# Optimization experiments

Hardware: AMD Instinct MI355X
Metric: run time of the kernel (lower is better)

## Reference

```python
import jax, jax.numpy as jnp
import numpy as np

B, T_Q, T_K, H = 16, 1024, 1024, 1024


def _linear_params(key, fan_in, fan_out):
    kw, kb = jax.random.split(key)
    bound = 1.0 / np.sqrt(fan_in)
    W = jax.random.uniform(kw, (fan_out, fan_in), jnp.float32, -bound, bound)
    b = jax.random.uniform(kb, (fan_out,), jnp.float32, -bound, bound)
    return W, b


def setup_inputs() -> dict:
    key = jax.random.key(0)
    ks = jax.random.split(key, 6)
    query = jax.random.normal(ks[0], (B, T_Q, H), jnp.float32)
    keys = jax.random.normal(ks[1], (B, T_K, H), jnp.float32)
    values = jax.random.normal(ks[2], (B, T_K, H), jnp.float32)
    Wq, bq = _linear_params(ks[3], H, H)
    Wk, bk = _linear_params(ks[4], H, H)
    Wo, bo = _linear_params(ks[5], H, H)
    return {"query": query, "keys": keys, "values": values,
            "Wq": Wq, "bq": bq, "Wk": Wk, "bk": bk, "Wo": Wo, "bo": bo}


def reference(query, keys, values, Wq, bq, Wk, bk, Wo, bo):
    # Linear projections (torch Linear: x @ W.T + b)
    q = jnp.einsum('bth,oh->bto', query, Wq) + bq   # (B, T_Q, H)
    k = jnp.einsum('bsh,oh->bso', keys, Wk) + bk    # (B, T_K, H)
    # Unscaled scores -> softmax over key axis (dropout is identity at eval)
    scores = jnp.einsum('bto,bso->bts', q, k)       # (B, T_Q, T_K)
    attn = jax.nn.softmax(scores, axis=-1)
    ctx = jnp.einsum('bts,bsh->bth', attn, values)  # note: raw values, value_fc unused in source
    ctx = ctx / jnp.sqrt(jnp.float32(values.shape[1]))
    out = jnp.einsum('bth,oh->bto', ctx, Wo) + bo
    return out
```

## Files before the change

### kernel.cpp

```cpp
#include <hip/hip_runtime.h>
#include <math.h>

typedef __attribute__((ext_vector_type(4))) float f32x4;
typedef __attribute__((ext_vector_type(8))) _Float16 h16x8;
typedef __attribute__((ext_vector_type(4))) short s16x4;

__device__ inline unsigned short f2h(float f) {
    union { _Float16 h; unsigned short u; } v; v.h = (_Float16)f; return v.u;
}

__device__ inline void async16(const void* g, void* l) {
    __builtin_amdgcn_global_load_lds(
        (const __attribute__((address_space(1))) unsigned int*)g,
        (__attribute__((address_space(3))) unsigned int*)l, 16, 0, 0);
}

#define BM 256
#define BN 256
#define BK 64
#define NTHREADS 512


__device__ inline void stage_half(const unsigned short* g, int row0, int kel, int K,
                                  unsigned ldsbase, char* smem, int tid) {
    const int rl  = tid >> 3;
    const int scb = ((tid & 7) ^ (rl & 7)) << 4;
    char* wb = smem + ldsbase + (unsigned)((tid >> 6) << 10);
#pragma unroll
    for (int s = 0; s < 2; ++s) {
        long off = ((long)(row0 + s * 64 + rl) * K + kel) * 2 + scb;
        async16((const char*)g + off, wb + s * 8192);
    }
}

__device__ inline h16x8 ld_frag(const char* smem, unsigned base, int row, int kbyte) {
    unsigned off = base + (unsigned)(row * 128) + (unsigned)(kbyte ^ ((row & 7) << 4));
    return *(const h16x8*)(smem + off);
}

template<int OM>
__global__ __launch_bounds__(NTHREADS, 2)
void gemm256(const unsigned short* __restrict__ A,
             const unsigned short* __restrict__ B,
             const float* __restrict__ bias,
             void* __restrict__ C, int N, int K,
             long sA, long sB, long sC, float scale)
{
    __shared__ __align__(16) char smem[131072];

    const int tid  = threadIdx.x;
    const int wv   = tid >> 6;
    const int lane = tid & 63;
    const int wr = wv >> 2, wc = wv & 3;
    const int lrow = lane & 15;
    const int kq16 = (lane >> 4) * 16;

    const long gx = gridDim.x, gy = gridDim.y;
    const long nwg = gx * gy * (long)gridDim.z;
    const long hw  = ((long)blockIdx.z * gy + blockIdx.y) * gx + blockIdx.x;
    const long qq = nwg >> 3, rr = nwg & 7;
    const long xcd = hw & 7, pos = hw >> 3;
    const long lg = (xcd < rr) ? xcd * (qq + 1) + pos
                               : rr * (qq + 1) + (xcd - rr) * qq + pos;
    const int bx = (int)(lg % gx);
    const long rem = lg / gx;
    const int by = (int)(rem % gy);
    const int bz = (int)(rem / gy);

    const int n0 = bx * BN;
    const int m0 = by * BM;

    const unsigned short* Ag = A + (long)bz * sA;
    const unsigned short* Bg = B + (long)bz * sB;

    const int NT = K / BK;

    auto stageA = [&](int t, int h) {
        stage_half(Ag, m0 + h * 128, t * BK, K,
                   (unsigned)(((t & 1) << 16) + (h << 14)), smem, tid);
    };
    auto stageB = [&](int t, int h) {
        stage_half(Bg, n0 + h * 128, t * BK, K,
                   (unsigned)(((t & 1) << 16) + 32768 + (h << 14)), smem, tid);
    };

    f32x4 acc[8][4];
#pragma unroll
    for (int i = 0; i < 8; ++i)
#pragma unroll
        for (int j = 0; j < 4; ++j) acc[i][j] = (f32x4){0.f, 0.f, 0.f, 0.f};

    const unsigned AbaseW = (unsigned)(wr * 16384);
    const unsigned BbaseW = (unsigned)(32768 + (wc >> 1) * 16384);
    const int brow0 = (wc & 1) * 64;

    stageB(0, 0); stageB(0, 1); stageA(0, 0); stageA(0, 1); stageB(1, 0); stageB(1, 1);
    asm volatile("s_waitcnt vmcnt(4)" ::: "memory");
    __builtin_amdgcn_sched_barrier(0);
    __builtin_amdgcn_s_barrier();

    h16x8 bfr[4][2], afr[2][2];

    for (int i = 0; i < NT / 2; ++i) {
        const int t1 = 2 * i + 1, t2 = 2 * i + 2, t3 = 2 * i + 3;
#pragma unroll
        for (int q = 0; q < 4; ++q) {
            if (q == 0) {
#pragma unroll
                for (int j = 0; j < 4; ++j)
#pragma unroll
                    for (int ks = 0; ks < 2; ++ks)
                        bfr[j][ks] = ld_frag(smem, BbaseW, brow0 + j * 16 + lrow, ks * 64 + kq16);
            }
#pragma unroll
            for (int f = 0; f < 2; ++f)
#pragma unroll
                for (int ks = 0; ks < 2; ++ks)
                    afr[f][ks] = ld_frag(smem, AbaseW, q * 32 + f * 16 + lrow, ks * 64 + kq16);
            if (q == 0)      stageA(t1, 0);
            else if (q == 1) stageA(t1, 1);
            else if (q == 2) { if (t2 < NT) stageB(t2, 0); }
            else             { if (t2 < NT) stageB(t2, 1); }

            __builtin_amdgcn_s_barrier();
            asm volatile("s_waitcnt lgkmcnt(0)" ::: "memory");
            __builtin_amdgcn_sched_barrier(0);
            __builtin_amdgcn_s_setprio(1);
#pragma unroll
            for (int f = 0; f < 2; ++f)
#pragma unroll
                for (int j = 0; j < 4; ++j)
#pragma unroll
                    for (int ks = 0; ks < 2; ++ks)
                        acc[2 * q + f][j] = __builtin_amdgcn_mfma_f32_16x16x32_f16(
                            afr[f][ks], bfr[j][ks], acc[2 * q + f][j], 0, 0, 0);
            __builtin_amdgcn_s_setprio(0);
            if (q == 3) {
                if (t2 < NT) { asm volatile("s_waitcnt vmcnt(4)" ::: "memory"); }
                else         { asm volatile("s_waitcnt vmcnt(0)" ::: "memory"); }
                __builtin_amdgcn_sched_barrier(0);
            }
            __builtin_amdgcn_s_barrier();
        }
#pragma unroll
        for (int q = 0; q < 4; ++q) {
            if (q == 0) {
#pragma unroll
                for (int j = 0; j < 4; ++j)
#pragma unroll
                    for (int ks = 0; ks < 2; ++ks)
                        bfr[j][ks] = ld_frag(smem, 65536u + BbaseW, brow0 + j * 16 + lrow, ks * 64 + kq16);
            }
#pragma unroll
            for (int f = 0; f < 2; ++f)
#pragma unroll
                for (int ks = 0; ks < 2; ++ks)
                    afr[f][ks] = ld_frag(smem, 65536u + AbaseW, q * 32 + f * 16 + lrow, ks * 64 + kq16);
            if (q == 0)      { if (t2 < NT) stageA(t2, 0); }
            else if (q == 1) { if (t2 < NT) stageA(t2, 1); }
            else if (q == 2) { if (t3 < NT) stageB(t3, 0); }
            else             { if (t3 < NT) stageB(t3, 1); }

            __builtin_amdgcn_s_barrier();
            asm volatile("s_waitcnt lgkmcnt(0)" ::: "memory");
            __builtin_amdgcn_sched_barrier(0);
            __builtin_amdgcn_s_setprio(1);
#pragma unroll
            for (int f = 0; f < 2; ++f)
#pragma unroll
                for (int j = 0; j < 4; ++j)
#pragma unroll
                    for (int ks = 0; ks < 2; ++ks)
                        acc[2 * q + f][j] = __builtin_amdgcn_mfma_f32_16x16x32_f16(
                            afr[f][ks], bfr[j][ks], acc[2 * q + f][j], 0, 0, 0);
            __builtin_amdgcn_s_setprio(0);
            if (q == 3) {
                if (t3 < NT) { asm volatile("s_waitcnt vmcnt(4)" ::: "memory"); }
                else         { asm volatile("s_waitcnt vmcnt(0)" ::: "memory"); }
                __builtin_amdgcn_sched_barrier(0);
            }
            __builtin_amdgcn_s_barrier();
        }
    }

#pragma unroll
    for (int j = 0; j < 4; ++j) {
        const int col = n0 + wc * 64 + j * 16 + lrow;
        const float bb = bias ? bias[col] : 0.f;
#pragma unroll
        for (int mi = 0; mi < 8; ++mi) {
#pragma unroll
            for (int r = 0; r < 4; ++r) {
                const long row = m0 + wr * 128 + mi * 16 + (lane >> 4) * 4 + r;
                const float v = acc[mi][j][r] * scale + bb;
                const long idx = (long)bz * sC + row * (long)N + col;
                if constexpr (OM == 0) ((float*)C)[idx] = v;
                else                   ((unsigned short*)C)[idx] = f2h(v);
            }
        }
    }
}

__global__ __launch_bounds__(256)
void conv_f16(const float* __restrict__ in, unsigned short* __restrict__ out, int n)
{
    int i = (blockIdx.x * 256 + threadIdx.x) * 4;
    if (i >= n) return;
    float4 v = *(const float4*)(in + i);
    s16x4 o = {(short)f2h(v.x), (short)f2h(v.y), (short)f2h(v.z), (short)f2h(v.w)};
    *(s16x4*)(out + i) = o;
}

__global__ __launch_bounds__(256)
void transpose_f16(const float* __restrict__ in, unsigned short* __restrict__ out)
{
    __shared__ float tile[32][33];
    const long base = (long)blockIdx.z * 1024 * 1024;
    const int h0 = blockIdx.x * 32, t0 = blockIdx.y * 32;
    for (int i = threadIdx.y; i < 32; i += 8)
        tile[i][threadIdx.x] = in[base + (long)(t0 + i) * 1024 + h0 + threadIdx.x];
    __syncthreads();
    for (int i = threadIdx.y; i < 32; i += 8)
        out[base + (long)(h0 + i) * 1024 + t0 + threadIdx.x] = f2h(tile[threadIdx.x][i]);
}

__global__ __launch_bounds__(256)
void softmax_f16(const float* __restrict__ S, unsigned short* __restrict__ P)
{
    long row = blockIdx.x;
    const int tid = threadIdx.x;
    float4 v = *(const float4*)(S + row * 1024 + tid * 4);
    float m = fmaxf(fmaxf(v.x, v.y), fmaxf(v.z, v.w));
#pragma unroll
    for (int off = 1; off < 64; off <<= 1) m = fmaxf(m, __shfl_xor(m, off));
    __shared__ float redm[4];
    int wave = tid >> 6, lane = tid & 63;
    if (lane == 0) redm[wave] = m;
    __syncthreads();
    m = fmaxf(fmaxf(redm[0], redm[1]), fmaxf(redm[2], redm[3]));

    float e0 = expf(v.x - m), e1 = expf(v.y - m), e2 = expf(v.z - m), e3 = expf(v.w - m);
    float s = e0 + e1 + e2 + e3;
#pragma unroll
    for (int off = 1; off < 64; off <<= 1) s += __shfl_xor(s, off);
    __shared__ float reds[4];
    if (lane == 0) reds[wave] = s;
    __syncthreads();
    s = reds[0] + reds[1] + reds[2] + reds[3];
    float inv = 1.f / s;
    s16x4 o = {(short)f2h(e0 * inv), (short)f2h(e1 * inv),
               (short)f2h(e2 * inv), (short)f2h(e3 * inv)};
    *(s16x4*)(P + row * 1024 + tid * 4) = o;
}

extern "C" void kernel_launch(void* const* d_in, const int* in_sizes, int n_in,
                              void* d_out, int out_size, void* d_ws, size_t ws_size,
                              hipStream_t stream)
{
    const float* query  = (const float*)d_in[0];
    const float* keys   = (const float*)d_in[1];
    const float* values = (const float*)d_in[2];
    const float* Wq     = (const float*)d_in[3];
    const float* bq     = (const float*)d_in[4];
    const float* Wk     = (const float*)d_in[5];
    const float* bk     = (const float*)d_in[6];
    const float* Wo     = (const float*)d_in[7];
    const float* bo     = (const float*)d_in[8];

    const int  T = 1024, H = 1024;
    const long NE = 16384L * 1024;
    const long NW = 1024L * 1024;

    size_t need = (size_t)(NE * 5 + NW * 3) * sizeof(unsigned short);
    if (ws_size < need) return;

    unsigned short* ws  = (unsigned short*)d_ws;
    unsigned short* Xq  = ws;
    unsigned short* Xk  = Xq + NE;
    unsigned short* qf  = Xk + NE;
    unsigned short* kf  = qf + NE;
    unsigned short* vT  = kf + NE;
    unsigned short* Wqh = vT + NE;
    unsigned short* Wkh = Wqh + NW;
    unsigned short* Woh = Wkh + NW;
    unsigned short* attn = Xq;
    unsigned short* ctx  = Xk;
    float* scores = (float*)d_out;

    conv_f16<<<16384, 256, 0, stream>>>(query, Xq, (int)NE);
    conv_f16<<<16384, 256, 0, stream>>>(keys,  Xk, (int)NE);
    conv_f16<<<1024,  256, 0, stream>>>(Wq, Wqh, (int)NW);
    conv_f16<<<1024,  256, 0, stream>>>(Wk, Wkh, (int)NW);
    conv_f16<<<1024,  256, 0, stream>>>(Wo, Woh, (int)NW);
    transpose_f16<<<dim3(32, 32, 16), dim3(32, 8), 0, stream>>>(values, vT);

    gemm256<1><<<dim3(4, 64, 1), NTHREADS, 0, stream>>>(
        Xq, Wqh, bq, qf, H, H, 0, 0, 0, 1.f);
    gemm256<1><<<dim3(4, 64, 1), NTHREADS, 0, stream>>>(
        Xk, Wkh, bk, kf, H, H, 0, 0, 0, 1.f);
    gemm256<0><<<dim3(4, 4, 16), NTHREADS, 0, stream>>>(
        qf, kf, nullptr, scores, T, H, (long)T * H, (long)T * H, (long)T * T, 1.f);
    softmax_f16<<<16384, 256, 0, stream>>>(scores, attn);
    gemm256<1><<<dim3(4, 4, 16), NTHREADS, 0, stream>>>(
        attn, vT, nullptr, ctx, H, T, (long)T * T, (long)T * H, (long)T * H, 1.f / 32.f);
    gemm256<0><<<dim3(4, 64, 1), NTHREADS, 0, stream>>>(
        ctx, Woh, bo, d_out, H, H, 0, 0, 0, 1.f);
}
```

Measured before the change: 317.5 us.

## Restructure GEMM main loop to one barrier per K-tile with register double-buffered A fragments

Replaces the hand-interleaved two-tile loop, which staged global loads across quarter steps and placed barriers around every MFMA group, with a simpler per-tile loop. The whole next tile is issued at the start of each iteration, and A fragments are double-buffered in registers so the next quarter's LDS reads overlap the current MFMAs. It is meant to remove three of the four workgroup barriers per quarter step. In exchange, each tile waits for vmcnt(0), so the full next-tile global load must finish within one tile of compute, and the prefetch depth drops from a staggered 1.5 tiles.

```diff
diff --git a/kernel.cpp b/kernel.cpp
--- a/kernel.cpp
+++ b/kernel.cpp
@@ -94,37 +94,46 @@
     const unsigned BbaseW = (unsigned)(32768 + (wc >> 1) * 16384);
     const int brow0 = (wc & 1) * 64;
 
-    stageB(0, 0); stageB(0, 1); stageA(0, 0); stageA(0, 1); stageB(1, 0); stageB(1, 1);
-    asm volatile("s_waitcnt vmcnt(4)" ::: "memory");
+    stageB(0, 0); stageB(0, 1); stageA(0, 0); stageA(0, 1);
+    asm volatile("s_waitcnt vmcnt(0)" ::: "memory");
     __builtin_amdgcn_sched_barrier(0);
     __builtin_amdgcn_s_barrier();
 
-    h16x8 bfr[4][2], afr[2][2];
-
-    for (int i = 0; i < NT / 2; ++i) {
-        const int t1 = 2 * i + 1, t2 = 2 * i + 2, t3 = 2 * i + 3;
+    h16x8 bfr[4][2];
+    h16x8 afr[2][2][2];
+
+    for (int t = 0; t < NT; ++t) {
+        const unsigned buf = (unsigned)((t & 1) << 16);
+
+#pragma unroll
+        for (int j = 0; j < 4; ++j)
+#pragma unroll
+            for (int ks = 0; ks < 2; ++ks)
+                bfr[j][ks] = ld_frag(smem, buf + BbaseW, brow0 + j * 16 + lrow, ks * 64 + kq16);
+#pragma unroll
+        for (int f = 0; f < 2; ++f)
+#pragma unroll
+            for (int ks = 0; ks < 2; ++ks)
+                afr[0][f][ks] = ld_frag(smem, buf + AbaseW, f * 16 + lrow, ks * 64 + kq16);
+
+        if (t + 1 < NT) {
+            stageB(t + 1, 0); stageB(t + 1, 1);
+            stageA(t + 1, 0); stageA(t + 1, 1);
+        }
+
 #pragma unroll
         for (int q = 0; q < 4; ++q) {
-            if (q == 0) {
-#pragma unroll
-                for (int j = 0; j < 4; ++j)
-#pragma unroll
-                    for (int ks = 0; ks < 2; ++ks)
-                        bfr[j][ks] = ld_frag(smem, BbaseW, brow0 + j * 16 + lrow, ks * 64 + kq16);
-            }
-#pragma unroll
-            for (int f = 0; f < 2; ++f)
-#pragma unroll
-                for (int ks = 0; ks < 2; ++ks)
-                    afr[f][ks] = ld_frag(smem, AbaseW, q * 32 + f * 16 + lrow, ks * 64 + kq16);
-            if (q == 0)      stageA(t1, 0);
-            else if (q == 1) stageA(t1, 1);
-            else if (q == 2) { if (t2 < NT) stageB(t2, 0); }
-            else             { if (t2 < NT) stageB(t2, 1); }
-
-            __builtin_amdgcn_s_barrier();
             asm volatile("s_waitcnt lgkmcnt(0)" ::: "memory");
             __builtin_amdgcn_sched_barrier(0);
+            if (q < 3) {
+#pragma unroll
+                for (int f = 0; f < 2; ++f)
+#pragma unroll
+                    for (int ks = 0; ks < 2; ++ks)
+                        afr[(q + 1) & 1][f][ks] =
+                            ld_frag(smem, buf + AbaseW, (q + 1) * 32 + f * 16 + lrow, ks * 64 + kq16);
+            }
+            __builtin_amdgcn_sched_barrier(0);
             __builtin_amdgcn_s_setprio(1);
 #pragma unroll
             for (int f = 0; f < 2; ++f)
@@ -133,54 +142,14 @@
 #pragma unroll
                     for (int ks = 0; ks < 2; ++ks)
                         acc[2 * q + f][j] = __builtin_amdgcn_mfma_f32_16x16x32_f16(
-                            afr[f][ks], bfr[j][ks], acc[2 * q + f][j], 0, 0, 0);
+                            afr[q & 1][f][ks], bfr[j][ks], acc[2 * q + f][j], 0, 0, 0);
             __builtin_amdgcn_s_setprio(0);
-            if (q == 3) {
-                if (t2 < NT) { asm volatile("s_waitcnt vmcnt(4)" ::: "memory"); }
-                else         { asm volatile("s_waitcnt vmcnt(0)" ::: "memory"); }
-                __builtin_amdgcn_sched_barrier(0);
-            }
-            __builtin_amdgcn_s_barrier();
+            __builtin_amdgcn_sched_barrier(0);
         }
-#pragma unroll
-        for (int q = 0; q < 4; ++q) {
-            if (q == 0) {
-#pragma unroll
-                for (int j = 0; j < 4; ++j)
-#pragma unroll
-                    for (int ks = 0; ks < 2; ++ks)
-                        bfr[j][ks] = ld_frag(smem, 65536u + BbaseW, brow0 + j * 16 + lrow, ks * 64 + kq16);
-            }
-#pragma unroll
-            for (int f = 0; f < 2; ++f)
-#pragma unroll
-                for (int ks = 0; ks < 2; ++ks)
-                    afr[f][ks] = ld_frag(smem, 65536u + AbaseW, q * 32 + f * 16 + lrow, ks * 64 + kq16);
-            if (q == 0)      { if (t2 < NT) stageA(t2, 0); }
-            else if (q == 1) { if (t2 < NT) stageA(t2, 1); }
-            else if (q == 2) { if (t3 < NT) stageB(t3, 0); }
-            else             { if (t3 < NT) stageB(t3, 1); }
-
-            __builtin_amdgcn_s_barrier();
-            asm volatile("s_waitcnt lgkmcnt(0)" ::: "memory");
-            __builtin_amdgcn_sched_barrier(0);
-            __builtin_amdgcn_s_setprio(1);
-#pragma unroll
-            for (int f = 0; f < 2; ++f)
-#pragma unroll
-                for (int j = 0; j < 4; ++j)
-#pragma unroll
-                    for (int ks = 0; ks < 2; ++ks)
-                        acc[2 * q + f][j] = __builtin_amdgcn_mfma_f32_16x16x32_f16(
-                            afr[f][ks], bfr[j][ks], acc[2 * q + f][j], 0, 0, 0);
-            __builtin_amdgcn_s_setprio(0);
-            if (q == 3) {
-                if (t3 < NT) { asm volatile("s_waitcnt vmcnt(4)" ::: "memory"); }
-                else         { asm volatile("s_waitcnt vmcnt(0)" ::: "memory"); }
-                __builtin_amdgcn_sched_barrier(0);
-            }
-            __builtin_amdgcn_s_barrier();
-        }
+
+        if (t + 1 < NT) { asm volatile("s_waitcnt vmcnt(0)" ::: "memory"); }
+        __builtin_amdgcn_sched_barrier(0);
+        __builtin_amdgcn_s_barrier();
     }
 
 #pragma unroll
```

After: 321.1 us. No clear change (+1.1%).

## Fuse fp32-to-fp16 input conversion into projection GEMM and store scores as fp16

Applied to the files above, without the earlier changes.

Adds a GEMM variant that loads the fp32 query/keys through registers, converts them to fp16 and writes them into swizzled LDS. This removes the two large standalone conversion kernels and their round trip through memory. The QK^T scores are now written as fp16 and softmaxed in place, which halves the score write and read traffic. The cost is fp16 range and precision on the unscaled scores, plus a register-staged A path with a full vmcnt(0) wait every K-step that may hurt the projection pipeline. The main GEMM loop is also folded into a half-loop with the MFMA order changed.

```diff
diff --git a/kernel.cpp b/kernel.cpp
--- a/kernel.cpp
+++ b/kernel.cpp
@@ -7,6 +7,9 @@
 
 __device__ inline unsigned short f2h(float f) {
     union { _Float16 h; unsigned short u; } v; v.h = (_Float16)f; return v.u;
+}
+__device__ inline float h2f(unsigned short u) {
+    union { unsigned short u; _Float16 h; } v; v.u = u; return (float)v.h;
 }
 
 __device__ inline void async16(const void* g, void* l) {
@@ -36,6 +39,20 @@
 __device__ inline h16x8 ld_frag(const char* smem, unsigned base, int row, int kbyte) {
     unsigned off = base + (unsigned)(row * 128) + (unsigned)(kbyte ^ ((row & 7) << 4));
     return *(const h16x8*)(smem + off);
+}
+
+__device__ inline void xcd_swizzle(int& bx, int& by, int& bz) {
+    const long gx = gridDim.x, gy = gridDim.y;
+    const long nwg = gx * gy * (long)gridDim.z;
+    const long hw  = ((long)blockIdx.z * gy + blockIdx.y) * gx + blockIdx.x;
+    const long qq = nwg >> 3, rr = nwg & 7;
+    const long xcd = hw & 7, pos = hw >> 3;
+    const long lg = (xcd < rr) ? xcd * (qq + 1) + pos
+                               : rr * (qq + 1) + (xcd - rr) * qq + pos;
+    bx = (int)(lg % gx);
+    const long rem = lg / gx;
+    by = (int)(rem % gy);
+    bz = (int)(rem / gy);
 }
 
 template<int OM>
@@ -55,24 +72,12 @@
     const int lrow = lane & 15;
     const int kq16 = (lane >> 4) * 16;
 
-    const long gx = gridDim.x, gy = gridDim.y;
-    const long nwg = gx * gy * (long)gridDim.z;
-    const long hw  = ((long)blockIdx.z * gy + blockIdx.y) * gx + blockIdx.x;
-    const long qq = nwg >> 3, rr = nwg & 7;
-    const long xcd = hw & 7, pos = hw >> 3;
-    const long lg = (xcd < rr) ? xcd * (qq + 1) + pos
-                               : rr * (qq + 1) + (xcd - rr) * qq + pos;
-    const int bx = (int)(lg % gx);
-    const long rem = lg / gx;
-    const int by = (int)(rem % gy);
-    const int bz = (int)(rem / gy);
-
+    int bx, by, bz; xcd_swizzle(bx, by, bz);
     const int n0 = bx * BN;
     const int m0 = by * BM;
 
     const unsigned short* Ag = A + (long)bz * sA;
     const unsigned short* Bg = B + (long)bz * sB;
-
     const int NT = K / BK;
 
     auto stageA = [&](int t, int h) {
@@ -96,7 +101,6 @@
 
     stageB(0, 0); stageB(0, 1); stageA(0, 0); stageA(0, 1); stageB(1, 0); stageB(1, 1);
     asm volatile("s_waitcnt vmcnt(4)" ::: "memory");
-    __builtin_amdgcn_sched_barrier(0);
     __builtin_amdgcn_s_barrier();
 
     h16x8 bfr[4][2], afr[2][2];
@@ -104,82 +108,54 @@
     for (int i = 0; i < NT / 2; ++i) {
         const int t1 = 2 * i + 1, t2 = 2 * i + 2, t3 = 2 * i + 3;
 #pragma unroll
-        for (int q = 0; q < 4; ++q) {
-            if (q == 0) {
-#pragma unroll
-                for (int j = 0; j < 4; ++j)
+        for (int half = 0; half < 2; ++half) {
+            const unsigned hb = half ? 65536u : 0u;
+#pragma unroll
+            for (int q = 0; q < 4; ++q) {
+                if (q == 0) {
+#pragma unroll
+                    for (int j = 0; j < 4; ++j)
+#pragma unroll
+                        for (int ks = 0; ks < 2; ++ks)
+                            bfr[j][ks] = ld_frag(smem, hb + BbaseW, brow0 + j * 16 + lrow, ks * 64 + kq16);
+                }
+#pragma unroll
+                for (int f = 0; f < 2; ++f)
 #pragma unroll
                     for (int ks = 0; ks < 2; ++ks)
-                        bfr[j][ks] = ld_frag(smem, BbaseW, brow0 + j * 16 + lrow, ks * 64 + kq16);
+                        afr[f][ks] = ld_frag(smem, hb + AbaseW, q * 32 + f * 16 + lrow, ks * 64 + kq16);
+                if (half == 0) {
+                    if (q == 0)      stageA(t1, 0);
+                    else if (q == 1) stageA(t1, 1);
+                    else if (q == 2) { if (t2 < NT) stageB(t2, 0); }
+                    else             { if (t2 < NT) stageB(t2, 1); }
+                } else {
+                    if (q == 0)      { if (t2 < NT) stageA(t2, 0); }
+                    else if (q == 1) { if (t2 < NT) stageA(t2, 1); }
+                    else if (q == 2) { if (t3 < NT) stageB(t3, 0); }
+                    else             { if (t3 < NT) stageB(t3, 1); }
+                }
+
+                __builtin_amdgcn_s_barrier();
+                asm volatile("s_waitcnt lgkmcnt(0)" ::: "memory");
+                __builtin_amdgcn_sched_barrier(0);
+                __builtin_amdgcn_s_setprio(1);
+#pragma unroll
+                for (int ks = 0; ks < 2; ++ks)
+#pragma unroll
+                    for (int f = 0; f < 2; ++f)
+#pragma unroll
+                        for (int j = 0; j < 4; ++j)
+                            acc[2 * q + f][j] = __builtin_amdgcn_mfma_f32_16x16x32_f16(
+                                afr[f][ks], bfr[j][ks], acc[2 * q + f][j], 0, 0, 0);
+                __builtin_amdgcn_s_setprio(0);
+                if (q == 3) {
+                    const int tn = half ? t3 : t2;
+                    if (tn < NT) { asm volatile("s_waitcnt vmcnt(4)" ::: "memory"); }
+                    else         { asm volatile("s_waitcnt vmcnt(0)" ::: "memory"); }
+                }
+                __builtin_amdgcn_s_barrier();
             }
-#pragma unroll
-            for (int f = 0; f < 2; ++f)
-#pragma unroll
-                for (int ks = 0; ks < 2; ++ks)
-                    afr[f][ks] = ld_frag(smem, AbaseW, q * 32 + f * 16 + lrow, ks * 64 + kq16);
-            if (q == 0)      stageA(t1, 0);
-            else if (q == 1) stageA(t1, 1);
-            else if (q == 2) { if (t2 < NT) stageB(t2, 0); }
-            else             { if (t2 < NT) stageB(t2, 1); }
-
-            __builtin_amdgcn_s_barrier();
-            asm volatile("s_waitcnt lgkmcnt(0)" ::: "memory");
-            __builtin_amdgcn_sched_barrier(0);
-            __builtin_amdgcn_s_setprio(1);
-#pragma unroll
-            for (int f = 0; f < 2; ++f)
-#pragma unroll
-                for (int j = 0; j < 4; ++j)
-#pragma unroll
-                    for (int ks = 0; ks < 2; ++ks)
-                        acc[2 * q + f][j] = __builtin_amdgcn_mfma_f32_16x16x32_f16(
-                            afr[f][ks], bfr[j][ks], acc[2 * q + f][j], 0, 0, 0);
-            __builtin_amdgcn_s_setprio(0);
-            if (q == 3) {
-                if (t2 < NT) { asm volatile("s_waitcnt vmcnt(4)" ::: "memory"); }
-                else         { asm volatile("s_waitcnt vmcnt(0)" ::: "memory"); }
-                __builtin_amdgcn_sched_barrier(0);
-            }
-            __builtin_amdgcn_s_barrier();
-        }
-#pragma unroll
-        for (int q = 0; q < 4; ++q) {
-            if (q == 0) {
-#pragma unroll
-                for (int j = 0; j < 4; ++j)
-#pragma unroll
-                    for (int ks = 0; ks < 2; ++ks)
-                        bfr[j][ks] = ld_frag(smem, 65536u + BbaseW, brow0 + j * 16 + lrow, ks * 64 + kq16);
-            }
-#pragma unroll
-            for (int f = 0; f < 2; ++f)
-#pragma unroll
-                for (int ks = 0; ks < 2; ++ks)
-                    afr[f][ks] = ld_frag(smem, 65536u + AbaseW, q * 32 + f * 16 + lrow, ks * 64 + kq16);
-            if (q == 0)      { if (t2 < NT) stageA(t2, 0); }
-            else if (q == 1) { if (t2 < NT) stageA(t2, 1); }
-            else if (q == 2) { if (t3 < NT) stageB(t3, 0); }
-            else             { if (t3 < NT) stageB(t3, 1); }
-
-            __builtin_amdgcn_s_barrier();
-            asm volatile("s_waitcnt lgkmcnt(0)" ::: "memory");
-            __builtin_amdgcn_sched_barrier(0);
-            __builtin_amdgcn_s_setprio(1);
-#pragma unroll
-            for (int f = 0; f < 2; ++f)
-#pragma unroll
-                for (int j = 0; j < 4; ++j)
-#pragma unroll
-                    for (int ks = 0; ks < 2; ++ks)
-                        acc[2 * q + f][j] = __builtin_amdgcn_mfma_f32_16x16x32_f16(
-                            afr[f][ks], bfr[j][ks], acc[2 * q + f][j], 0, 0, 0);
-            __builtin_amdgcn_s_setprio(0);
-            if (q == 3) {
-                if (t3 < NT) { asm volatile("s_waitcnt vmcnt(4)" ::: "memory"); }
-                else         { asm volatile("s_waitcnt vmcnt(0)" ::: "memory"); }
-                __builtin_amdgcn_sched_barrier(0);
-            }
-            __builtin_amdgcn_s_barrier();
         }
     }
 
@@ -196,6 +172,133 @@
                 const long idx = (long)bz * sC + row * (long)N + col;
                 if constexpr (OM == 0) ((float*)C)[idx] = v;
                 else                   ((unsigned short*)C)[idx] = f2h(v);
+            }
+        }
+    }
+}
+
+__global__ __launch_bounds__(NTHREADS, 2)
+void gemm256_f32a(const float* __restrict__ A,
+                  const unsigned short* __restrict__ B,
+                  const float* __restrict__ bias,
+                  unsigned short* __restrict__ C, int N, int K)
+{
+    __shared__ __align__(16) char smem[131072];
+
+    const int tid  = threadIdx.x;
+    const int wv   = tid >> 6;
+    const int lane = tid & 63;
+    const int wr = wv >> 2, wc = wv & 3;
+    const int lrow = lane & 15;
+    const int kq16 = (lane >> 4) * 16;
+
+    int bx, by, bz; xcd_swizzle(bx, by, bz);
+    const int n0 = bx * BN;
+    const int m0 = by * BM;
+    const int NT = K / BK;
+
+    const int fm  = (tid >> 4);
+    const int c4  = tid & 15;
+
+    auto loadA = [&](int t, float4* r) {
+#pragma unroll
+        for (int l = 0; l < 8; ++l) {
+            int m = fm + l * 32;
+            r[l] = *(const float4*)(A + (long)(m0 + m) * K + t * BK + c4 * 4);
+        }
+    };
+    auto writeA = [&](int t, const float4* r) {
+        const unsigned buf = (unsigned)((t & 1) << 16);
+#pragma unroll
+        for (int l = 0; l < 8; ++l) {
+            int m = fm + l * 32;
+            int h = m >> 7, ri = m & 127;
+            unsigned addr = buf + (unsigned)(h * 16384 + ri * 128 +
+                              ((((c4 >> 1) ^ (ri & 7))) << 4) + ((c4 & 1) << 3));
+            float4 v = r[l];
+            s16x4 hv = {(short)f2h(v.x), (short)f2h(v.y), (short)f2h(v.z), (short)f2h(v.w)};
+            *(s16x4*)(smem + addr) = hv;
+        }
+    };
+    auto stageB = [&](int t, int h) {
+        stage_half(B, n0 + h * 128, t * BK, K,
+                   (unsigned)(((t & 1) << 16) + 32768 + (h << 14)), smem, tid);
+    };
+
+    f32x4 acc[8][4];
+#pragma unroll
+    for (int i = 0; i < 8; ++i)
+#pragma unroll
+        for (int j = 0; j < 4; ++j) acc[i][j] = (f32x4){0.f, 0.f, 0.f, 0.f};
+
+    const unsigned AbaseW = (unsigned)(wr * 16384);
+    const unsigned BbaseW = (unsigned)(32768 + (wc >> 1) * 16384);
+    const int brow0 = (wc & 1) * 64;
+
+    float4 a_pre[8];
+    loadA(0, a_pre);
+    asm volatile("s_waitcnt vmcnt(0)" ::: "memory");
+    writeA(0, a_pre);
+    stageB(0, 0); stageB(0, 1);
+    if (NT > 1) loadA(1, a_pre);
+    asm volatile("s_waitcnt lgkmcnt(0) vmcnt(8)" ::: "memory");
+    __builtin_amdgcn_s_barrier();
+
+    h16x8 bfr[4][2], afr[2][2];
+
+    for (int t = 0; t < NT; ++t) {
+        const unsigned buf = (unsigned)((t & 1) << 16);
+        if (t > 0) {
+            writeA(t, a_pre);
+            asm volatile("s_waitcnt lgkmcnt(0)" ::: "memory");
+            __builtin_amdgcn_s_barrier();
+        }
+#pragma unroll
+        for (int q = 0; q < 4; ++q) {
+            if (q == 0) {
+#pragma unroll
+                for (int j = 0; j < 4; ++j)
+#pragma unroll
+                    for (int ks = 0; ks < 2; ++ks)
+                        bfr[j][ks] = ld_frag(smem, buf + BbaseW, brow0 + j * 16 + lrow, ks * 64 + kq16);
+            }
+#pragma unroll
+            for (int f = 0; f < 2; ++f)
+#pragma unroll
+                for (int ks = 0; ks < 2; ++ks)
+                    afr[f][ks] = ld_frag(smem, buf + AbaseW, q * 32 + f * 16 + lrow, ks * 64 + kq16);
+            if (t + 1 < NT) {
+                if (q == 0) { stageB(t + 1, 0); loadA(t + 1, a_pre); }
+                else if (q == 1) stageB(t + 1, 1);
+            }
+            __builtin_amdgcn_s_barrier();
+            asm volatile("s_waitcnt lgkmcnt(0)" ::: "memory");
+            __builtin_amdgcn_sched_barrier(0);
+            __builtin_amdgcn_s_setprio(1);
+#pragma unroll
+            for (int ks = 0; ks < 2; ++ks)
+#pragma unroll
+                for (int f = 0; f < 2; ++f)
+#pragma unroll
+                    for (int j = 0; j < 4; ++j)
+                        acc[2 * q + f][j] = __builtin_amdgcn_mfma_f32_16x16x32_f16(
+                            afr[f][ks], bfr[j][ks], acc[2 * q + f][j], 0, 0, 0);
+            __builtin_amdgcn_s_setprio(0);
+            if (q == 3) { asm volatile("s_waitcnt vmcnt(0)" ::: "memory"); }
+            __builtin_amdgcn_s_barrier();
+        }
+    }
+
+#pragma unroll
+    for (int j = 0; j < 4; ++j) {
+        const int col = n0 + wc * 64 + j * 16 + lrow;
+        const float bb = bias[col];
+#pragma unroll
+        for (int mi = 0; mi < 8; ++mi) {
+#pragma unroll
+            for (int r = 0; r < 4; ++r) {
+                const long row = m0 + wr * 128 + mi * 16 + (lane >> 4) * 4 + r;
+                C[row * (long)N + col] = f2h(acc[mi][j][r] + bb);
             }
         }
     }
@@ -225,12 +328,14 @@
 }
 
 __global__ __launch_bounds__(256)
-void softmax_f16(const float* __restrict__ S, unsigned short* __restrict__ P)
+void softmax_ip(unsigned short* __restrict__ S)
 {
     long row = blockIdx.x;
     const int tid = threadIdx.x;
-    float4 v = *(const float4*)(S + row * 1024 + tid * 4);
-    float m = fmaxf(fmaxf(v.x, v.y), fmaxf(v.z, v.w));
+    s16x4 raw = *(s16x4*)(S + row * 1024 + tid * 4);
+    float v0 = h2f((unsigned short)raw[0]), v1 = h2f((unsigned short)raw[1]);
+    float v2 = h2f((unsigned short)raw[2]), v3 = h2f((unsigned short)raw[3]);
+    float m = fmaxf(fmaxf(v0, v1), fmaxf(v2, v3));
 #pragma unroll
     for (int off = 1; off < 64; off <<= 1) m = fmaxf(m, __shfl_xor(m, off));
     __shared__ float redm[4];
@@ -239,7 +344,7 @@
     __syncthreads();
     m = fmaxf(fmaxf(redm[0], redm[1]), fmaxf(redm[2], redm[3]));
 
-    float e0 = expf(v.x - m), e1 = expf(v.y - m), e2 = expf(v.z - m), e3 = expf(v.w - m);
+    float e0 = expf(v0 - m), e1 = expf(v1 - m), e2 = expf(v2 - m), e3 = expf(v3 - m);
     float s = e0 + e1 + e2 + e3;
 #pragma unroll
     for (int off = 1; off < 64; off <<= 1) s += __shfl_xor(s, off);
@@ -250,7 +355,7 @@
     float inv = 1.f / s;
     s16x4 o = {(short)f2h(e0 * inv), (short)f2h(e1 * inv),
                (short)f2h(e2 * inv), (short)f2h(e3 * inv)};
-    *(s16x4*)(P + row * 1024 + tid * 4) = o;
+    *(s16x4*)(S + row * 1024 + tid * 4) = o;
 }
 
 extern "C" void kernel_launch(void* const* d_in, const int* in_sizes, int n_in,
@@ -275,34 +380,27 @@
     if (ws_size < need) return;
 
     unsigned short* ws  = (unsigned short*)d_ws;
-    unsigned short* Xq  = ws;
-    unsigned short* Xk  = Xq + NE;
-    unsigned short* qf  = Xk + NE;
+    unsigned short* qf  = ws;
     unsigned short* kf  = qf + NE;
     unsigned short* vT  = kf + NE;
-    unsigned short* Wqh = vT + NE;
+    unsigned short* sc  = vT + NE;
+    unsigned short* ctx = sc + NE;
+    unsigned short* Wqh = ctx + NE;
     unsigned short* Wkh = Wqh + NW;
     unsigned short* Woh = Wkh + NW;
-    unsigned short* attn = Xq;
-    unsigned short* ctx  = Xk;
-    float* scores = (float*)d_out;
-
-    conv_f16<<<16384, 256, 0, stream>>>(query, Xq, (int)NE);
-    conv_f16<<<16384, 256, 0, stream>>>(keys,  Xk, (int)NE);
-    conv_f16<<<1024,  256, 0, stream>>>(Wq, Wqh, (int)NW);
-    conv_f16<<<1024,  256, 0, stream>>>(Wk, Wkh, (int)NW);
-    conv_f16<<<1024,  256, 0, stream>>>(Wo, Woh, (int)NW);
+
+    conv_f16<<<1024, 256, 0, stream>>>(Wq, Wqh, (int)NW);
+    conv_f16<<<1024, 256, 0, stream>>>(Wk, Wkh, (int)NW);
+    conv_f16<<<1024, 256, 0, stream>>>(Wo, Woh, (int)NW);
     transpose_f16<<<dim3(32, 32, 16), dim3(32, 8), 0, stream>>>(values, vT);
 
-    gemm256<1><<<dim3(4, 64, 1), NTHREADS, 0, stream>>>(
-        Xq, Wqh, bq, qf, H, H, 0, 0, 0, 1.f);
-    gemm256<1><<<dim3(4, 64, 1), NTHREADS, 0, stream>>>(
-        Xk, Wkh, bk, kf, H, H, 0, 0, 0, 1.f);
-    gemm256<0><<<dim3(4, 4, 16), NTHREADS, 0, stream>>>(
-        qf, kf, nullptr, scores, T, H, (long)T * H, (long)T * H, (long)T * T, 1.f);
-    softmax_f16<<<16384, 256, 0, stream>>>(scores, attn);
+    gemm256_f32a<<<dim3(4, 64, 1), NTHREADS, 0, stream>>>(query, Wqh, bq, qf, H, H);
+    gemm256_f32a<<<dim3(4, 64, 1), NTHREADS, 0, stream>>>(keys, Wkh, bk, kf, H, H);
     gemm256<1><<<dim3(4, 4, 16), NTHREADS, 0, stream>>>(
-        attn, vT, nullptr, ctx, H, T, (long)T * T, (long)T * H, (long)T * H, 1.f / 32.f);
+        qf, kf, nullptr, sc, T, H, (long)T * H, (long)T * H, (long)T * T, 1.f);
+    softmax_ip<<<16384, 256, 0, stream>>>(sc);
+    gemm256<1><<<dim3(4, 4, 16), NTHREADS, 0, stream>>>(
+        sc, vT, nullptr, ctx, H, T, (long)T * T, (long)T * H, (long)T * H, 1.f / 32.f);
     gemm256<0><<<dim3(4, 64, 1), NTHREADS, 0, stream>>>(
         ctx, Woh, bo, d_out, H, H, 0, 0, 0, 1.f);
 }
```

Result: no change. 320.3 us (+0.9%).
